# Kernel optimization log

Hardware: AMD Instinct MI355X
Metric: run time of the kernel (lower is better)

## Reference

```python
import jax, jax.numpy as jnp
from jax import lax
import numpy as np

P = 32      # num_series
H = 128     # hidden units
B = 32      # batch
T = 256     # sequence length

def setup_inputs() -> dict:
    key = jax.random.key(0)
    ks = jax.random.split(key, 8)
    s = 1.0 / np.sqrt(H)
    X     = jax.random.normal(ks[0], (B, T, P), dtype=jnp.float32)
    # per-network LSTM weights, PyTorch gate order (i, f, g, o) stacked in 4H
    W_ih  = jax.random.uniform(ks[1], (P, 4 * H, P), dtype=jnp.float32, minval=-s, maxval=s)
    W_hh  = jax.random.uniform(ks[2], (P, 4 * H, H), dtype=jnp.float32, minval=-s, maxval=s)
    b_ih  = jax.random.uniform(ks[3], (P, 4 * H), dtype=jnp.float32, minval=-s, maxval=s)
    b_hh  = jax.random.uniform(ks[4], (P, 4 * H), dtype=jnp.float32, minval=-s, maxval=s)
    # Conv1d(hidden, 1, kernel_size=1) == per-timestep linear H -> 1, per network
    W_out = jax.random.uniform(ks[5], (P, H), dtype=jnp.float32, minval=-s, maxval=s)
    b_out = jax.random.uniform(ks[6], (P,), dtype=jnp.float32, minval=-s, maxval=s)
    return {"X": X, "W_ih": W_ih, "W_hh": W_hh, "b_ih": b_ih,
            "b_hh": b_hh, "W_out": W_out, "b_out": b_out}

def reference(X, W_ih, W_hh, b_ih, b_hh, W_out, b_out):
    # X: (B, T, P); p independent 1-layer LSTMs run on the same input,
    # batched along a network axis n (size P) with distinct weights.
    # Precompute input projections for all steps/networks: (T, B, P, 4H)
    xproj = jnp.einsum('btd,nkd->tbnk', X, W_ih) + b_ih + b_hh

    def step(carry, xp_t):
        h, c = carry                                   # (B, P, H) each
        gates = xp_t + jnp.einsum('bnh,nkh->bnk', h, W_hh)
        i, f, g, o = jnp.split(gates, 4, axis=-1)
        i = jax.nn.sigmoid(i)
        f = jax.nn.sigmoid(f)
        g = jnp.tanh(g)
        o = jax.nn.sigmoid(o)
        c = f * c + i * g
        h = o * jnp.tanh(c)
        return (h, c), h

    h0 = jnp.zeros((X.shape[0], W_ih.shape[0], W_hh.shape[2]), X.dtype)
    (_, _), hs = lax.scan(step, (h0, h0), xproj)        # hs: (T, B, P, H)
    # 1x1 conv head per network, then concat over networks -> (B, T, P)
    pred = jnp.einsum('tbnh,nh->btn', hs, W_out) + b_out
    return pred
```

## Files before the change

### kernel.cpp

```cpp
#include <hip/hip_runtime.h>
#include <stdint.h>

#define NP 32
#define NH 128
#define NB 32
#define NT 256
#define FH 512

typedef __attribute__((ext_vector_type(4))) float float4_t;
typedef __attribute__((ext_vector_type(8))) __bf16 bf16x8;

static __device__ __forceinline__ float4_t mfma_bf16(bf16x8 a, bf16x8 b, float4_t c) {
  return __builtin_amdgcn_mfma_f32_16x16x32_bf16(a, b, c, 0, 0, 0);
}

#define LOG2E 1.4426950408889634f

#define BAR() __asm__ volatile("s_waitcnt lgkmcnt(0)\n\ts_barrier" ::: "memory")

__global__ __launch_bounds__(512, 1) void clstm_fused(
    const float* __restrict__ X, const float* __restrict__ Wih,
    const float* __restrict__ Whh, const float* __restrict__ bih,
    const float* __restrict__ bhh, const float* __restrict__ Wout,
    const float* __restrict__ bout, float* __restrict__ out)
{
  const int net = blockIdx.x >> 3, bq = blockIdx.x & 7;
  const int tid = threadIdx.x;
  const int w = tid >> 6, lane = tid & 63;
  const int quad = lane >> 4, l16 = lane & 15;

  __shared__ __bf16 hfrag[2][4][4][4][8];

  {
    ((int*)hfrag)[tid] = 0;
  }
  __syncthreads();

  bf16x8 bfrag[4][5];
  float4_t bias4[4];
#pragma unroll
  for (int g = 0; g < 4; ++g) {
    const float scale = (g == 2) ? (-2.0f*LOG2E) : (-LOG2E);
    const int col = g*NH + w*16 + l16;
#pragma unroll
    for (int kc = 0; kc < 5; ++kc) {
      const float* src = (kc == 0) ? (Wih + ((size_t)net*FH + col)*NP + quad*8)
                                   : (Whh + ((size_t)net*FH + col)*NH + (kc-1)*32 + quad*8);
      bf16x8 bf;
#pragma unroll
      for (int j = 0; j < 8; ++j) bf[j] = (__bf16)(src[j] * scale);
      bfrag[g][kc] = bf;
    }
    const float b = (bih[net*FH + col] + bhh[net*FH + col]) * scale;
    bias4[g] = (float4_t){b, b, b, b};
  }

  bf16x8 wof[4];
#pragma unroll
  for (int kc = 0; kc < 4; ++kc) {
    const float* wp = Wout + net*NH + kc*32 + quad*8;
#pragma unroll
    for (int j = 0; j < 8; ++j) wof[kc][j] = (__bf16)wp[j];
  }
  const float bo = bout[net];

  float cs = 0.f;
  const float S2 = -2.0f*LOG2E;

  const float* xrow = X + (size_t)(bq*4 + (l16 & 3))*(NT*NP) + quad*8;

  const int kcp = w >> 1, q2 = ((w & 1) << 1) | (l16 >> 3), jj = l16 & 7;

  float* outp = out + ((size_t)bq*4)*(NT*NP) + net;

  bf16x8 ax;
  {
    float xv0[8];
    *(float4_t*)&xv0[0] = *(const float4_t*)xrow;
    *(float4_t*)&xv0[4] = *(const float4_t*)(xrow + 4);
#pragma unroll
    for (int j = 0; j < 8; ++j) ax[j] = (__bf16)xv0[j];
  }
  const float* xp = xrow + NP;
  float xv[8] = {0.f,0.f,0.f,0.f,0.f,0.f,0.f,0.f};

  for (int t = 0; t < NT; ++t) {
    const int rd = t & 1, wr = rd ^ 1;

    bf16x8 ah[4];
#pragma unroll
    for (int kc = 0; kc < 4; ++kc)
      ah[kc] = *(const bf16x8*)&hfrag[rd][kc][quad][l16 & 3][0];

    float4_t accx[4];
#pragma unroll
    for (int g = 0; g < 4; ++g)
      accx[g] = mfma_bf16(ax, bfrag[g][0], bias4[g]);

    if (t + 1 < NT) {
      *(float4_t*)&xv[0] = *(const float4_t*)xp;
      *(float4_t*)&xv[4] = *(const float4_t*)(xp + 4);
    }

    float4_t acc[4];
#pragma unroll
    for (int g = 0; g < 4; ++g) {
      float4_t a0 = mfma_bf16(ah[0], bfrag[g][1], accx[g]);
      float4_t a1 = mfma_bf16(ah[2], bfrag[g][3], (float4_t){0.f,0.f,0.f,0.f});
      a0 = mfma_bf16(ah[1], bfrag[g][2], a0);
      a1 = mfma_bf16(ah[3], bfrag[g][4], a1);
      acc[g] = a0 + a1;
    }

    float gv[4];
#pragma unroll
    for (int g = 0; g < 4; ++g) {
      float a01 = (quad & 1) ? acc[g][1] : acc[g][0];
      float a23 = (quad & 1) ? acc[g][3] : acc[g][2];
      gv[g] = (quad & 2) ? a23 : a01;
    }

    float h;
    {
      float ei = __builtin_amdgcn_exp2f(gv[0]);
      float ig = __builtin_amdgcn_rcpf(1.0f + ei);
      float ef = __builtin_amdgcn_exp2f(gv[1]);
      float fg = __builtin_amdgcn_rcpf(1.0f + ef);
      float eg = __builtin_amdgcn_exp2f(fminf(gv[2], 126.0f));
      float rg = __builtin_amdgcn_rcpf(1.0f + eg);
      float t0 = S2 * rg;
      float gg2 = t0 - t0 * eg;
      float eo = __builtin_amdgcn_exp2f(gv[3]);
      float og = __builtin_amdgcn_rcpf(1.0f + eo);
      cs = fg * cs + ig * gg2;
      float ec = __builtin_amdgcn_exp2f(fminf(cs, 126.0f));
      float rc = __builtin_amdgcn_rcpf(1.0f + ec);
      float th = rc - ec * rc;
      h = og * th;
    }

    hfrag[wr][kcp][q2][quad][jj] = (__bf16)h;

    if (w == 0 && t > 0) {
      float4_t p0 = {bo, bo, bo, bo};
      float4_t p1 = {0.f, 0.f, 0.f, 0.f};
      p0 = mfma_bf16(ah[0], wof[0], p0);
      p1 = mfma_bf16(ah[2], wof[2], p1);
      p0 = mfma_bf16(ah[1], wof[1], p0);
      p1 = mfma_bf16(ah[3], wof[3], p1);
      float4_t po = p0 + p1;
      if (lane == 0) {
#pragma unroll
        for (int r = 0; r < 4; ++r)
          outp[(size_t)r*(NT*NP) + (t - 1)*NP] = po[r];
      }
    }

#pragma unroll
    for (int j = 0; j < 8; ++j) ax[j] = (__bf16)xv[j];
    xp += NP;

    BAR();
  }

  if (w == 0) {
    bf16x8 ahf[4];
#pragma unroll
    for (int kc = 0; kc < 4; ++kc)
      ahf[kc] = *(const bf16x8*)&hfrag[NT & 1][kc][quad][l16 & 3][0];
    float4_t p0 = {bo, bo, bo, bo};
    float4_t p1 = {0.f, 0.f, 0.f, 0.f};
    p0 = mfma_bf16(ahf[0], wof[0], p0);
    p1 = mfma_bf16(ahf[2], wof[2], p1);
    p0 = mfma_bf16(ahf[1], wof[1], p0);
    p1 = mfma_bf16(ahf[3], wof[3], p1);
    float4_t po = p0 + p1;
    if (lane == 0) {
#pragma unroll
      for (int r = 0; r < 4; ++r)
        outp[(size_t)r*(NT*NP) + (NT - 1)*NP] = po[r];
    }
  }
}

extern "C" void kernel_launch(void* const* d_in, const int* in_sizes, int n_in,
                              void* d_out, int out_size, void* d_ws, size_t ws_size,
                              hipStream_t stream) {
  const float* X    = (const float*)d_in[0];
  const float* Wih  = (const float*)d_in[1];
  const float* Whh  = (const float*)d_in[2];
  const float* bih  = (const float*)d_in[3];
  const float* bhh  = (const float*)d_in[4];
  const float* Wout = (const float*)d_in[5];
  const float* bout = (const float*)d_in[6];
  float* out = (float*)d_out;
  (void)in_sizes; (void)n_in; (void)out_size; (void)d_ws; (void)ws_size;

  clstm_fused<<<256, 512, 0, stream>>>(X, Wih, Whh, bih, bhh, Wout, bout, out);
}
```

Measured before the change: 256.3 us.

## Split batch across twice as many blocks and defer output head to epilogue

The recurrent kernel now handles 2 batch rows per block instead of 4, launching 512 blocks with a waves-per-eu hint so two blocks can share a CU. X is pre-converted to bf16 by a separate kernel. Hidden states are written to workspace each step and the 1x1 output head is computed after the time loop instead of inside the serial step. This shortens the per-step critical path and doubles parallelism, at the cost of an extra launch, a large workspace write stream, and half the MFMA rows going unused. A fallback path is kept for when the workspace is too small.

```diff
diff --git a/kernel.cpp b/kernel.cpp
--- a/kernel.cpp
+++ b/kernel.cpp
@@ -9,6 +9,7 @@
 
 typedef __attribute__((ext_vector_type(4))) float float4_t;
 typedef __attribute__((ext_vector_type(8))) __bf16 bf16x8;
+typedef __attribute__((ext_vector_type(4))) __bf16 bf16x4;
 
 static __device__ __forceinline__ float4_t mfma_bf16(bf16x8 a, bf16x8 b, float4_t c) {
   return __builtin_amdgcn_mfma_f32_16x16x32_bf16(a, b, c, 0, 0, 0);
@@ -18,26 +19,39 @@
 
 #define BAR() __asm__ volatile("s_waitcnt lgkmcnt(0)\n\ts_barrier" ::: "memory")
 
-__global__ __launch_bounds__(512, 1) void clstm_fused(
-    const float* __restrict__ X, const float* __restrict__ Wih,
+
+__global__ __launch_bounds__(512, 1) void xcvt(
+    const float* __restrict__ X, __bf16* __restrict__ Xb)
+{
+  const int i = (blockIdx.x * 512 + threadIdx.x) * 4;
+  float4_t v = *(const float4_t*)(X + i);
+  bf16x4 o;
+#pragma unroll
+  for (int j = 0; j < 4; ++j) o[j] = (__bf16)v[j];
+  *(bf16x4*)(Xb + i) = o;
+}
+
+__global__ __attribute__((amdgpu_flat_work_group_size(512, 512),
+                          amdgpu_waves_per_eu(4, 4)))
+void clstm_fused2(
+    const __bf16* __restrict__ Xb, const float* __restrict__ Wih,
     const float* __restrict__ Whh, const float* __restrict__ bih,
     const float* __restrict__ bhh, const float* __restrict__ Wout,
-    const float* __restrict__ bout, float* __restrict__ out)
+    const float* __restrict__ bout, float* __restrict__ out,
+    __bf16* __restrict__ wsH)
 {
-  const int net = blockIdx.x >> 3, bq = blockIdx.x & 7;
+  const int net = blockIdx.x >> 4, bq = blockIdx.x & 15;
   const int tid = threadIdx.x;
   const int w = tid >> 6, lane = tid & 63;
   const int quad = lane >> 4, l16 = lane & 15;
 
   __shared__ __bf16 hfrag[2][4][4][4][8];
 
-  {
-    ((int*)hfrag)[tid] = 0;
-  }
+  { ((int*)hfrag)[tid] = 0; }
   __syncthreads();
 
   bf16x8 bfrag[4][5];
-  float4_t bias4[4];
+  float bsc[4];
 #pragma unroll
   for (int g = 0; g < 4; ++g) {
     const float scale = (g == 2) ? (-2.0f*LOG2E) : (-LOG2E);
@@ -51,38 +65,21 @@
       for (int j = 0; j < 8; ++j) bf[j] = (__bf16)(src[j] * scale);
       bfrag[g][kc] = bf;
     }
-    const float b = (bih[net*FH + col] + bhh[net*FH + col]) * scale;
-    bias4[g] = (float4_t){b, b, b, b};
-  }
-
-  bf16x8 wof[4];
-#pragma unroll
-  for (int kc = 0; kc < 4; ++kc) {
-    const float* wp = Wout + net*NH + kc*32 + quad*8;
-#pragma unroll
-    for (int j = 0; j < 8; ++j) wof[kc][j] = (__bf16)wp[j];
-  }
-  const float bo = bout[net];
+    bsc[g] = (bih[net*FH + col] + bhh[net*FH + col]) * scale;
+  }
 
   float cs = 0.f;
   const float S2 = -2.0f*LOG2E;
 
-  const float* xrow = X + (size_t)(bq*4 + (l16 & 3))*(NT*NP) + quad*8;
+  int xoff = (bq*2 + (l16 & 1))*(NT*NP) + quad*8;
 
   const int kcp = w >> 1, q2 = ((w & 1) << 1) | (l16 >> 3), jj = l16 & 7;
-
-  float* outp = out + ((size_t)bq*4)*(NT*NP) + net;
-
-  bf16x8 ax;
-  {
-    float xv0[8];
-    *(float4_t*)&xv0[0] = *(const float4_t*)xrow;
-    *(float4_t*)&xv0[4] = *(const float4_t*)(xrow + 4);
-#pragma unroll
-    for (int j = 0; j < 8; ++j) ax[j] = (__bf16)xv0[j];
-  }
-  const float* xp = xrow + NP;
-  float xv[8] = {0.f,0.f,0.f,0.f,0.f,0.f,0.f,0.f};
+  const int mrow = quad & 1;
+
+  int hoff = (blockIdx.x << 16) + quad*128 + w*16 + l16;
+
+  bf16x8 ax = *(const bf16x8*)(Xb + xoff);
+  xoff += NP;
 
   for (int t = 0; t < NT; ++t) {
     const int rd = t & 1, wr = rd ^ 1;
@@ -90,35 +87,24 @@
     bf16x8 ah[4];
 #pragma unroll
     for (int kc = 0; kc < 4; ++kc)
-      ah[kc] = *(const bf16x8*)&hfrag[rd][kc][quad][l16 & 3][0];
-
-    float4_t accx[4];
-#pragma unroll
-    for (int g = 0; g < 4; ++g)
-      accx[g] = mfma_bf16(ax, bfrag[g][0], bias4[g]);
+      ah[kc] = *(const bf16x8*)&hfrag[rd][kc][quad][l16 & 1][0];
+
+    float gv[4];
+#pragma unroll
+    for (int g = 0; g < 4; ++g) {
+      float4_t a0 = mfma_bf16(ax, bfrag[g][0], (float4_t){0.f,0.f,0.f,0.f});
+      float4_t a1 = mfma_bf16(ah[2], bfrag[g][3], (float4_t){0.f,0.f,0.f,0.f});
+      a0 = mfma_bf16(ah[0], bfrag[g][1], a0);
+      a1 = mfma_bf16(ah[3], bfrag[g][4], a1);
+      a0 = mfma_bf16(ah[1], bfrag[g][2], a0);
+      float4_t s = a0 + a1;
+      gv[g] = ((quad & 1) ? s[1] : s[0]) + bsc[g];
+    }
 
     if (t + 1 < NT) {
-      *(float4_t*)&xv[0] = *(const float4_t*)xp;
-      *(float4_t*)&xv[4] = *(const float4_t*)(xp + 4);
-    }
-
-    float4_t acc[4];
-#pragma unroll
-    for (int g = 0; g < 4; ++g) {
-      float4_t a0 = mfma_bf16(ah[0], bfrag[g][1], accx[g]);
-      float4_t a1 = mfma_bf16(ah[2], bfrag[g][3], (float4_t){0.f,0.f,0.f,0.f});
-      a0 = mfma_bf16(ah[1], bfrag[g][2], a0);
-      a1 = mfma_bf16(ah[3], bfrag[g][4], a1);
-      acc[g] = a0 + a1;
-    }
-
-    float gv[4];
-#pragma unroll
-    for (int g = 0; g < 4; ++g) {
-      float a01 = (quad & 1) ? acc[g][1] : acc[g][0];
-      float a23 = (quad & 1) ? acc[g][3] : acc[g][2];
-      gv[g] = (quad & 2) ? a23 : a01;
-    }
+      ax = *(const bf16x8*)(Xb + xoff);
+    }
+    xoff += NP;
 
     float h;
     {
@@ -139,8 +125,144 @@
       h = og * th;
     }
 
+    if (quad < 2) {
+      hfrag[wr][kcp][q2][mrow][jj] = (__bf16)h;
+      wsH[hoff] = (__bf16)h;
+    }
+    hoff += 256;
+
+    BAR();
+  }
+
+  __threadfence();
+  __syncthreads();
+  float* ldsW = (float*)&hfrag[0][0][0][0][0];
+  if (tid < NH) ldsW[tid] = Wout[net*NH + tid];
+  __syncthreads();
+
+  const int tt = tid >> 1, m = tid & 1;
+  const __bf16* hp = wsH + ((size_t)blockIdx.x << 16) + tt*256 + m*128;
+  float s = bout[net];
+#pragma unroll
+  for (int kc = 0; kc < 16; ++kc) {
+    bf16x8 h8 = *(const bf16x8*)(hp + kc*8);
+#pragma unroll
+    for (int j = 0; j < 8; ++j)
+      s += (float)h8[j] * ldsW[kc*8 + j];
+  }
+  out[(size_t)(bq*2 + m)*(NT*NP) + tt*NP + net] = s;
+}
+
+__global__ __launch_bounds__(512, 1) void clstm_fused_fb(
+    const float* __restrict__ X, const float* __restrict__ Wih,
+    const float* __restrict__ Whh, const float* __restrict__ bih,
+    const float* __restrict__ bhh, const float* __restrict__ Wout,
+    const float* __restrict__ bout, float* __restrict__ out)
+{
+  const int net = blockIdx.x >> 3, bq = blockIdx.x & 7;
+  const int tid = threadIdx.x;
+  const int w = tid >> 6, lane = tid & 63;
+  const int quad = lane >> 4, l16 = lane & 15;
+
+  __shared__ __bf16 hfrag[2][4][4][4][8];
+  { ((int*)hfrag)[tid] = 0; }
+  __syncthreads();
+
+  bf16x8 bfrag[4][5];
+  float4_t bias4[4];
+#pragma unroll
+  for (int g = 0; g < 4; ++g) {
+    const float scale = (g == 2) ? (-2.0f*LOG2E) : (-LOG2E);
+    const int col = g*NH + w*16 + l16;
+#pragma unroll
+    for (int kc = 0; kc < 5; ++kc) {
+      const float* src = (kc == 0) ? (Wih + ((size_t)net*FH + col)*NP + quad*8)
+                                   : (Whh + ((size_t)net*FH + col)*NH + (kc-1)*32 + quad*8);
+      bf16x8 bf;
+#pragma unroll
+      for (int j = 0; j < 8; ++j) bf[j] = (__bf16)(src[j] * scale);
+      bfrag[g][kc] = bf;
+    }
+    const float b = (bih[net*FH + col] + bhh[net*FH + col]) * scale;
+    bias4[g] = (float4_t){b, b, b, b};
+  }
+
+  bf16x8 wof[4];
+#pragma unroll
+  for (int kc = 0; kc < 4; ++kc) {
+    const float* wp = Wout + net*NH + kc*32 + quad*8;
+#pragma unroll
+    for (int j = 0; j < 8; ++j) wof[kc][j] = (__bf16)wp[j];
+  }
+  const float bo = bout[net];
+
+  float cs = 0.f;
+  const float S2 = -2.0f*LOG2E;
+
+  const float* xrow = X + (size_t)(bq*4 + (l16 & 3))*(NT*NP) + quad*8;
+  const int kcp = w >> 1, q2 = ((w & 1) << 1) | (l16 >> 3), jj = l16 & 7;
+  float* outp = out + ((size_t)bq*4)*(NT*NP) + net;
+
+  bf16x8 ax;
+  {
+    float xv0[8];
+    *(float4_t*)&xv0[0] = *(const float4_t*)xrow;
+    *(float4_t*)&xv0[4] = *(const float4_t*)(xrow + 4);
+#pragma unroll
+    for (int j = 0; j < 8; ++j) ax[j] = (__bf16)xv0[j];
+  }
+  const float* xp = xrow + NP;
+  float xv[8] = {0.f,0.f,0.f,0.f,0.f,0.f,0.f,0.f};
+
+  for (int t = 0; t < NT; ++t) {
+    const int rd = t & 1, wr = rd ^ 1;
+    bf16x8 ah[4];
+#pragma unroll
+    for (int kc = 0; kc < 4; ++kc)
+      ah[kc] = *(const bf16x8*)&hfrag[rd][kc][quad][l16 & 3][0];
+    float4_t accx[4];
+#pragma unroll
+    for (int g = 0; g < 4; ++g)
+      accx[g] = mfma_bf16(ax, bfrag[g][0], bias4[g]);
+    if (t + 1 < NT) {
+      *(float4_t*)&xv[0] = *(const float4_t*)xp;
+      *(float4_t*)&xv[4] = *(const float4_t*)(xp + 4);
+    }
+    float4_t acc[4];
+#pragma unroll
+    for (int g = 0; g < 4; ++g) {
+      float4_t a0 = mfma_bf16(ah[0], bfrag[g][1], accx[g]);
+      float4_t a1 = mfma_bf16(ah[2], bfrag[g][3], (float4_t){0.f,0.f,0.f,0.f});
+      a0 = mfma_bf16(ah[1], bfrag[g][2], a0);
+      a1 = mfma_bf16(ah[3], bfrag[g][4], a1);
+      acc[g] = a0 + a1;
+    }
+    float gv[4];
+#pragma unroll
+    for (int g = 0; g < 4; ++g) {
+      float a01 = (quad & 1) ? acc[g][1] : acc[g][0];
+      float a23 = (quad & 1) ? acc[g][3] : acc[g][2];
+      gv[g] = (quad & 2) ? a23 : a01;
+    }
+    float h;
+    {
+      float ei = __builtin_amdgcn_exp2f(gv[0]);
+      float ig = __builtin_amdgcn_rcpf(1.0f + ei);
+      float ef = __builtin_amdgcn_exp2f(gv[1]);
+      float fg = __builtin_amdgcn_rcpf(1.0f + ef);
+      float eg = __builtin_amdgcn_exp2f(fminf(gv[2], 126.0f));
+      float rg = __builtin_amdgcn_rcpf(1.0f + eg);
+      float t0 = S2 * rg;
+      float gg2 = t0 - t0 * eg;
+      float eo = __builtin_amdgcn_exp2f(gv[3]);
+      float og = __builtin_amdgcn_rcpf(1.0f + eo);
+      cs = fg * cs + ig * gg2;
+      float ec = __builtin_amdgcn_exp2f(fminf(cs, 126.0f));
+      float rc = __builtin_amdgcn_rcpf(1.0f + ec);
+      float th = rc - ec * rc;
+      h = og * th;
+    }
     hfrag[wr][kcp][q2][quad][jj] = (__bf16)h;
-
     if (w == 0 && t > 0) {
       float4_t p0 = {bo, bo, bo, bo};
       float4_t p1 = {0.f, 0.f, 0.f, 0.f};
@@ -155,11 +277,9 @@
           outp[(size_t)r*(NT*NP) + (t - 1)*NP] = po[r];
       }
     }
-
 #pragma unroll
     for (int j = 0; j < 8; ++j) ax[j] = (__bf16)xv[j];
     xp += NP;
-
     BAR();
   }
 
@@ -194,7 +314,17 @@
   const float* Wout = (const float*)d_in[5];
   const float* bout = (const float*)d_in[6];
   float* out = (float*)d_out;
-  (void)in_sizes; (void)n_in; (void)out_size; (void)d_ws; (void)ws_size;
-
-  clstm_fused<<<256, 512, 0, stream>>>(X, Wih, Whh, bih, bhh, Wout, bout, out);
-}
+  (void)in_sizes; (void)n_in; (void)out_size;
+
+  const size_t need = (size_t)NB*NT*NP*2 + (size_t)512*65536*2;
+  if (d_ws != nullptr && ws_size >= need) {
+    __bf16* wsX = (__bf16*)d_ws;
+    __bf16* wsH = wsX + (size_t)NB*NT*NP;
+    xcvt<<<128, 512, 0, stream>>>(X, wsX);
+    clstm_fused2<<<512, 512, 0, stream>>>(wsX, Wih, Whh, bih, bhh, Wout,
+                                          bout, out, wsH);
+  } else {
+    clstm_fused_fb<<<256, 512, 0, stream>>>(X, Wih, Whh, bih, bhh, Wout,
+                                            bout, out);
+  }
+}
```

New measurement: 405.3 us. 58.2% more time.
